# Performance work log

Measured on AMD Instinct MI355X. Metric: run time of the kernel, lower is better.

## Reference

```python
import jax, jax.numpy as jnp
import numpy as np

B, L, D = 256, 512, 768
ATTN_H, WIDTH_DIM = 1000, 20
BINS = jnp.array([1, 2, 3, 4, 5, 6, 7, 8, 12, 16, 20, 24, 32, 64, 128], dtype=jnp.int64)


def setup_inputs() -> dict:
    key = jax.random.key(0)
    ks = jax.random.split(key, 20)
    s = 0.02
    embeds = jax.random.normal(ks[0], (B, L, D), dtype=jnp.float32)
    spans = jnp.sort(jax.random.randint(ks[1], (B, 2), 0, L, dtype=jnp.int64), axis=1)
    inp = {
        "embeds": embeds,
        "spans": spans,
        # attention scorer: Linear(768,1000) -> LeakyReLU -> Linear(1000,1)
        "aw1": jax.random.normal(ks[2], (D, ATTN_H), dtype=jnp.float32) * s,
        "ab1": jnp.zeros((ATTN_H,), dtype=jnp.float32),
        "aw2": jax.random.normal(ks[3], (ATTN_H, 1), dtype=jnp.float32) * s,
        "ab2": jnp.zeros((1,), dtype=jnp.float32),
        # width embedding: [len(bins)+1 = 16, 20]
        "width_emb": jax.random.normal(ks[4], (16, WIDTH_DIM), dtype=jnp.float32) * s,
        # score MLP: 2324 -> 1024 -> 512 -> 256 -> 30
        "sw1": jax.random.normal(ks[5], (2324, 1024), dtype=jnp.float32) * s,
        "sb1": jnp.zeros((1024,), dtype=jnp.float32),
        "sw2": jax.random.normal(ks[6], (1024, 512), dtype=jnp.float32) * s,
        "sb2": jnp.zeros((512,), dtype=jnp.float32),
        "sw3": jax.random.normal(ks[7], (512, 256), dtype=jnp.float32) * s,
        "sb3": jnp.zeros((256,), dtype=jnp.float32),
        "sw4": jax.random.normal(ks[8], (256, 30), dtype=jnp.float32) * s,
        "sb4": jnp.zeros((30,), dtype=jnp.float32),
    }
    return inp


def reference(embeds, spans, aw1, ab1, aw2, ab2, width_emb,
              sw1, sb1, sw2, sb2, sw3, sb3, sw4, sb4):
    b, l, d = embeds.shape
    start, end = spans[:, 0], spans[:, 1]

    # gather start/end token embeds -> [B, 2*D]
    se = jnp.take_along_axis(embeds, spans[:, :, None], axis=1).reshape(b, 2 * d)

    # attention logits over all tokens: Linear -> LeakyReLU -> Linear
    h = jax.nn.leaky_relu(embeds @ aw1 + ab1)          # [B, L, 1000]
    attns = (h @ aw2 + ab2)[..., 0]                     # [B, L]

    # ragged per-span softmax pooling, vectorized via masking (inclusive span)
    cols = jnp.arange(l, dtype=spans.dtype)[None, :]
    mask = (cols >= start[:, None]) & (cols <= end[:, None])
    w = jax.nn.softmax(jnp.where(mask, attns, jnp.float32(-1e30)), axis=1)
    w = w * mask.astype(w.dtype)
    attn_embeds = jnp.einsum("bl,bld->bd", w, embeds)   # [B, D]

    # width bucket embedding
    widths = end - start + 1
    idx = jnp.sum(widths[:, None] > BINS[None, :], axis=1)
    wemb = width_emb[idx]                                # [B, 20]

    x = jnp.concatenate([se, attn_embeds, wemb], axis=1)  # [B, 2324]
    x = jax.nn.leaky_relu(x @ sw1 + sb1)
    x = jax.nn.leaky_relu(x @ sw2 + sb2)
    x = jax.nn.leaky_relu(x @ sw3 + sb3)
    return x @ sw4 + sb4                                  # [B, 30]
```

## Files before the change

### kernel.cpp

```cpp
#include <hip/hip_runtime.h>
#include <hip/hip_bf16.h>

#define B_   256
#define L_   512
#define D_   768
#define H_   1000
#define NPAD 1024
#define XDIM 2324
#define MAXPOS (B_*L_)

typedef _Float16 half8 __attribute__((ext_vector_type(8)));
typedef float    f32x4 __attribute__((ext_vector_type(4)));

__global__ __launch_bounds__(256) void scan_kernel(const int* __restrict__ spans,
                                                   int* __restrict__ meta) {
    int b = threadIdx.x;
    int s = spans[2 * b], e = spans[2 * b + 1];
    s = min(max(s, 0), L_ - 1);
    e = min(max(e, s), L_ - 1);
    int w = e - s + 1;
    __shared__ int sw[256];
    sw[b] = w;
    __syncthreads();
    for (int d = 1; d < 256; d <<= 1) {
        int v = 0;
        if (b >= d) v = sw[b - d];
        __syncthreads();
        if (b >= d) sw[b] += v;
        __syncthreads();
    }
    meta[b]       = sw[b] - w;
    meta[256 + b] = s;
    meta[512 + b] = e;
    if (b == 255) meta[768] = sw[255];
}

__global__ __launch_bounds__(256) void pos_fill(const int* __restrict__ meta,
                                                int* __restrict__ pos_list) {
    int b = blockIdx.x;
    int off = meta[b], start = meta[256 + b], end = meta[512 + b];
    int w = end - start + 1;
    for (int i = threadIdx.x; i < w; i += blockDim.x)
        pos_list[off + i] = (b << 16) | (start + i);
}

__global__ __launch_bounds__(256) void transpose_w(const float* __restrict__ aw1,
                                                   _Float16* __restrict__ WbT) {
    int k0 = blockIdx.x * 32, n0 = blockIdx.y * 32;
    int tx = threadIdx.x & 31, ty = threadIdx.x >> 5;
    __shared__ float T[32][33];
#pragma unroll
    for (int it = 0; it < 4; it++) {
        int k = k0 + ty + 8 * it;
        int n = n0 + tx;
        T[ty + 8 * it][tx] = (n < H_) ? aw1[(size_t)k * H_ + n] : 0.f;
    }
    __syncthreads();
#pragma unroll
    for (int it = 0; it < 4; it++) {
        int n = n0 + ty + 8 * it;
        WbT[(size_t)n * D_ + k0 + tx] = (_Float16)T[tx][ty + 8 * it];
    }
}

#define AP 776
__global__ __launch_bounds__(256) void attn_gemm_v2(
    const float* __restrict__ embeds, const _Float16* __restrict__ WbT,
    const float* __restrict__ ab1, const float* __restrict__ aw2,
    const int* __restrict__ pos_list, const int* __restrict__ meta,
    float* __restrict__ attns) {
    int npos = meta[768];
    int m0 = blockIdx.x * 32;
    if (m0 >= npos) return;
    int t = threadIdx.x;
    int lane = t & 63, w = t >> 6;
    int q = lane >> 4, l15 = lane & 15;

    __shared__ alignas(16) _Float16 As[32][AP];
    __shared__ unsigned rowoff[32];
    __shared__ float attns_s[4][32];

    if (t < 32) {
        unsigned off = 0;
        int m = m0 + t;
        if (m < npos) {
            int p = pos_list[m];
            off = (unsigned)((p >> 16) * (L_ * D_) + (p & 0xffff) * D_);
        }
        rowoff[t] = off;
    }
    __syncthreads();

    {
        int row = t >> 3;
        int cs = (t & 7) * 96;
        const float* src = embeds + rowoff[row] + cs;
#pragma unroll
        for (int i2 = 0; i2 < 12; i2++) {
            float4 v0 = *(const float4*)(src + i2 * 8);
            float4 v1 = *(const float4*)(src + i2 * 8 + 4);
            half8 h;
            h[0] = (_Float16)v0.x; h[1] = (_Float16)v0.y;
            h[2] = (_Float16)v0.z; h[3] = (_Float16)v0.w;
            h[4] = (_Float16)v1.x; h[5] = (_Float16)v1.y;
            h[6] = (_Float16)v1.z; h[7] = (_Float16)v1.w;
            *(half8*)&As[row][cs + i2 * 8] = h;
        }
    }
    __syncthreads();

    float pacc[2][4];
#pragma unroll
    for (int i = 0; i < 2; i++)
#pragma unroll
        for (int r = 0; r < 4; r++) pacc[i][r] = 0.f;

    for (int g = 0; g < 4; g++) {
        int colbase = w * 256 + g * 64;
        const _Float16* bbase = WbT + (size_t)(colbase + l15) * D_ + q * 8;
        f32x4 acc[2][4];
#pragma unroll
        for (int i = 0; i < 2; i++)
#pragma unroll
            for (int j = 0; j < 4; j++) acc[i][j] = (f32x4){0.f, 0.f, 0.f, 0.f};

        for (int k0 = 0; k0 < D_; k0 += 32) {
            half8 bf[4];
#pragma unroll
            for (int j = 0; j < 4; j++)
                bf[j] = *(const half8*)(bbase + (size_t)j * 16 * D_ + k0);
            half8 af[2];
#pragma unroll
            for (int i = 0; i < 2; i++)
                af[i] = *(const half8*)&As[l15 + 16 * i][k0 + q * 8];
#pragma unroll
            for (int i = 0; i < 2; i++)
#pragma unroll
                for (int j = 0; j < 4; j++)
                    acc[i][j] = __builtin_amdgcn_mfma_f32_16x16x32_f16(af[i], bf[j], acc[i][j], 0, 0, 0);
        }

        float bj[4], aj[4];
#pragma unroll
        for (int j = 0; j < 4; j++) {
            int col = colbase + j * 16 + l15;
            bool v = col < H_;
            bj[j] = v ? ab1[col] : 0.f;
            aj[j] = v ? aw2[col] : 0.f;
        }
#pragma unroll
        for (int i = 0; i < 2; i++) {
#pragma unroll
            for (int r = 0; r < 4; r++) {
                float p = 0.f;
#pragma unroll
                for (int j = 0; j < 4; j++) {
                    float h = acc[i][j][r] + bj[j];
                    h = h > 0.f ? h : 0.01f * h;
                    p += h * aj[j];
                }
                p += __shfl_xor(p, 1);
                p += __shfl_xor(p, 2);
                p += __shfl_xor(p, 4);
                p += __shfl_xor(p, 8);
                pacc[i][r] += p;
            }
        }
    }
    if (l15 == 0) {
#pragma unroll
        for (int i = 0; i < 2; i++)
#pragma unroll
            for (int r = 0; r < 4; r++)
                attns_s[w][i * 16 + q * 4 + r] = pacc[i][r];
    }
    __syncthreads();
    if (t < 32 && m0 + t < npos)
        attns[m0 + t] = attns_s[0][t] + attns_s[1][t] + attns_s[2][t] + attns_s[3][t];
}

__global__ __launch_bounds__(256) void build_x(
    const float* __restrict__ embeds, const float* __restrict__ attns,
    const int* __restrict__ meta, const float* __restrict__ width_emb,
    float* __restrict__ x) {
    int b = blockIdx.x, s = blockIdx.y, t = threadIdx.x;
    int off = meta[b], start = meta[256 + b], end = meta[512 + b];
    int w = end - start + 1;
    __shared__ float sv[512];
    __shared__ float red[256];
    for (int i = t; i < w; i += 256) sv[i] = attns[off + i];
    __syncthreads();
    float m = -3.0e38f;
    for (int i = t; i < w; i += 256) m = fmaxf(m, sv[i]);
    red[t] = m;
    __syncthreads();
    for (int st = 128; st > 0; st >>= 1) {
        if (t < st) red[t] = fmaxf(red[t], red[t + st]);
        __syncthreads();
    }
    float mx = red[0];
    __syncthreads();
    float ssum = 0.f;
    for (int i = t; i < w; i += 256) {
        float e = __expf(sv[i] - mx);
        sv[i] = e;
        ssum += e;
    }
    red[t] = ssum;
    __syncthreads();
    for (int st = 128; st > 0; st >>= 1) {
        if (t < st) red[t] += red[t + st];
        __syncthreads();
    }
    float inv = 1.0f / red[0];
    __syncthreads();

    int dim = s * 256 + t;
    const float* base = embeds + ((size_t)b * L_ + start) * D_ + dim;
    float acc = 0.f;
    int i = 0;
    for (; i + 3 < w; i += 4) {
        float w0 = sv[i], w1 = sv[i + 1], w2 = sv[i + 2], w3 = sv[i + 3];
        const float* p = base + (size_t)i * D_;
        acc += w0 * p[0] + w1 * p[D_] + w2 * p[2 * D_] + w3 * p[3 * D_];
    }
    for (; i < w; i++) acc += sv[i] * base[(size_t)i * D_];

    float* xb = x + (size_t)b * XDIM;
    xb[1536 + dim] = acc * inv;
    xb[dim]        = base[0];
    xb[768 + dim]  = embeds[((size_t)b * L_ + end) * D_ + dim];
    if (s == 0 && t < 20) {
        const int bins[15] = {1, 2, 3, 4, 5, 6, 7, 8, 12, 16, 20, 24, 32, 64, 128};
        int idx = 0;
#pragma unroll
        for (int q2 = 0; q2 < 15; q2++) idx += (w > bins[q2]);
        xb[2304 + t] = width_emb[idx * 20 + t];
    }
}

__global__ __launch_bounds__(256) void mlp_gemm_sk(
    const float* __restrict__ A, const float* __restrict__ W,
    float* __restrict__ out, int M, int N, int K, int kchunk) {
    __shared__ float As[16][68];
    __shared__ float Ws[16][64];
    int t = threadIdx.x;
    int tx = t & 15, ty = t >> 4;
    int m0 = blockIdx.x * 64, n0 = blockIdx.y * 64;
    int ks = blockIdx.z * kchunk;
    int ke = min(ks + kchunk, K);
    if (ks >= ke) return;
    int ar = t >> 2, akc = (t & 3) * 4;
    int wk = t >> 4, wnc = (t & 15) * 4;
    bool n4 = ((N & 3) == 0);

    float acc[4][4];
#pragma unroll
    for (int i = 0; i < 4; i++)
#pragma unroll
        for (int j = 0; j < 4; j++) acc[i][j] = 0.f;

    auto loadA = [&](int k0) -> float4 {
        float4 r = make_float4(0.f, 0.f, 0.f, 0.f);
        int k = k0 + akc;
        if (k < ke) r = *(const float4*)(A + (size_t)(m0 + ar) * K + k);
        return r;
    };
    auto loadW = [&](int k0) -> float4 {
        float4 r = make_float4(0.f, 0.f, 0.f, 0.f);
        int k = k0 + wk;
        if (k < ke) {
            int n = n0 + wnc;
            const float* p = W + (size_t)k * N + n;
            if (n4) {
                r = *(const float4*)p;
            } else {
                float tmp[4];
#pragma unroll
                for (int q2 = 0; q2 < 4; q2++)
                    tmp[q2] = (n + q2 < N) ? p[q2] : 0.f;
                r = make_float4(tmp[0], tmp[1], tmp[2], tmp[3]);
            }
        }
        return r;
    };

    float4 aR = loadA(ks), wR = loadW(ks);
    for (int k0 = ks; k0 < ke; k0 += 16) {
        As[akc + 0][ar] = aR.x;
        As[akc + 1][ar] = aR.y;
        As[akc + 2][ar] = aR.z;
        As[akc + 3][ar] = aR.w;
        *(float4*)&Ws[wk][wnc] = wR;
        __syncthreads();
        if (k0 + 16 < ke) { aR = loadA(k0 + 16); wR = loadW(k0 + 16); }
#pragma unroll
        for (int kk = 0; kk < 16; kk++) {
            float4 a = *(const float4*)&As[kk][ty * 4];
            float4 b = *(const float4*)&Ws[kk][tx * 4];
            float av[4] = {a.x, a.y, a.z, a.w};
            float bv[4] = {b.x, b.y, b.z, b.w};
#pragma unroll
            for (int i = 0; i < 4; i++)
#pragma unroll
                for (int j = 0; j < 4; j++) acc[i][j] += av[i] * bv[j];
        }
        __syncthreads();
    }
#pragma unroll
    for (int i = 0; i < 4; i++) {
#pragma unroll
        for (int j = 0; j < 4; j++) {
            int nn = n0 + tx * 4 + j;
            if (nn < N)
                atomicAdd(&out[(size_t)(m0 + ty * 4 + i) * N + nn], acc[i][j]);
        }
    }
}

__global__ __launch_bounds__(256) void bias_act(
    const float* __restrict__ src, const float* __restrict__ bias,
    float* __restrict__ dst, int total, int N, int leaky) {
    int i = blockIdx.x * 256 + threadIdx.x;
    int stride = gridDim.x * 256;
    for (; i < total; i += stride) {
        float v = src[i] + bias[i % N];
        if (leaky) v = v > 0.f ? v : 0.01f * v;
        dst[i] = v;
    }
}

extern "C" void kernel_launch(void* const* d_in, const int* in_sizes, int n_in,
                              void* d_out, int out_size, void* d_ws, size_t ws_size,
                              hipStream_t stream) {
    const float* embeds    = (const float*)d_in[0];
    const int*   spans     = (const int*)d_in[1];
    const float* aw1       = (const float*)d_in[2];
    const float* ab1       = (const float*)d_in[3];
    const float* aw2       = (const float*)d_in[4];
    const float* width_emb = (const float*)d_in[6];
    const float* sw1 = (const float*)d_in[7],  *sb1 = (const float*)d_in[8];
    const float* sw2 = (const float*)d_in[9],  *sb2 = (const float*)d_in[10];
    const float* sw3 = (const float*)d_in[11], *sb3 = (const float*)d_in[12];
    const float* sw4 = (const float*)d_in[13], *sb4 = (const float*)d_in[14];
    float* out = (float*)d_out;

    char* ws = (char*)d_ws;
    float*     attns    = (float*)ws;
    int*       pos_list = (int*)(ws + (size_t)MAXPOS * 4);
    int*       meta     = (int*)(ws + (size_t)MAXPOS * 8);
    _Float16*  WbT      = (_Float16*)(ws + (size_t)MAXPOS * 8 + 4096);
    float* x  = (float*)(ws + (size_t)MAXPOS * 8 + 4096 + (size_t)NPAD * D_ * 2);
    float* y1 = x + (size_t)B_ * XDIM;
    float* y2 = y1 + (size_t)B_ * 1024;
    float* y3 = y2 + (size_t)B_ * 512;
    float* y4 = y3 + (size_t)B_ * 256;
    size_t ybytes = ((size_t)B_ * (1024 + 512 + 256 + 30)) * 4;

    hipMemsetAsync(y1, 0, ybytes, stream);
    scan_kernel<<<1, 256, 0, stream>>>(spans, meta);
    pos_fill<<<B_, 256, 0, stream>>>(meta, pos_list);
    transpose_w<<<dim3(D_ / 32, NPAD / 32), 256, 0, stream>>>(aw1, WbT);
    attn_gemm_v2<<<MAXPOS / 32, 256, 0, stream>>>(
        embeds, WbT, ab1, aw2, pos_list, meta, attns);
    build_x<<<dim3(B_, 3), 256, 0, stream>>>(embeds, attns, meta, width_emb, x);

    mlp_gemm_sk<<<dim3(4, 16, 8), 256, 0, stream>>>(x,  sw1, y1, B_, 1024, XDIM, 292);
    bias_act<<<256, 256, 0, stream>>>(y1, sb1, y1, B_ * 1024, 1024, 1);
    mlp_gemm_sk<<<dim3(4, 8, 8), 256, 0, stream>>>(y1, sw2, y2, B_, 512, 1024, 128);
    bias_act<<<128, 256, 0, stream>>>(y2, sb2, y2, B_ * 512, 512, 1);
    mlp_gemm_sk<<<dim3(4, 4, 8), 256, 0, stream>>>(y2, sw3, y3, B_, 256, 512, 64);
    bias_act<<<64, 256, 0, stream>>>(y3, sb3, y3, B_ * 256, 256, 1);
    mlp_gemm_sk<<<dim3(4, 1, 8), 256, 0, stream>>>(y3, sw4, y4, B_, 30, 256, 32);
    bias_act<<<30, 256, 0, stream>>>(y4, sb4, out, B_ * 30, 30, 0);
}
```

Before: 901.7 us.

## Retile attention GEMM to 128x128 blocks with double-buffered LDS and direct global-to-LDS loads

The attention scorer GEMM changes from 32-row blocks that each sweep all 1024 hidden columns to 2D 128x128 tiles over positions and hidden columns. The K loop is double-buffered: weights go straight to LDS via global_load_lds, and embeds are converted to fp16 in registers. Per-tile partial logits are combined with atomicAdd into a zeroed attns buffer, replacing the old in-block reduction. This should raise reuse of B from LDS and improve MFMA utilization, at the cost of an extra memset, atomics, and re-reading A for each of the 8 column tiles.

```diff
diff --git a/kernel.cpp b/kernel.cpp
--- a/kernel.cpp
+++ b/kernel.cpp
@@ -63,24 +63,34 @@
     }
 }
 
-#define AP 776
-__global__ __launch_bounds__(256) void attn_gemm_v2(
+#define BM   128
+#define BN   128
+#define BKT  32
+#define NKST (D_ / BKT)
+
+#define GLD_LDS16(gsrc, ldst) \
+    __builtin_amdgcn_global_load_lds((const __attribute__((address_space(1))) void*)(gsrc), \
+                                     (__attribute__((address_space(3))) void*)(ldst), 16, 0, 0)
+
+__global__ __launch_bounds__(256) void attn_gemm_v3(
     const float* __restrict__ embeds, const _Float16* __restrict__ WbT,
     const float* __restrict__ ab1, const float* __restrict__ aw2,
     const int* __restrict__ pos_list, const int* __restrict__ meta,
     float* __restrict__ attns) {
     int npos = meta[768];
-    int m0 = blockIdx.x * 32;
+    int m0 = blockIdx.x * BM;
     if (m0 >= npos) return;
+    int n0 = blockIdx.y * BN;
     int t = threadIdx.x;
     int lane = t & 63, w = t >> 6;
     int q = lane >> 4, l15 = lane & 15;
-
-    __shared__ alignas(16) _Float16 As[32][AP];
-    __shared__ unsigned rowoff[32];
-    __shared__ float attns_s[4][32];
-
-    if (t < 32) {
+    int wr = w >> 1, wc = w & 1;
+
+    __shared__ alignas(16) _Float16 As[2][BM][BKT];
+    __shared__ alignas(16) _Float16 Bs[2][BN * BKT];
+    __shared__ unsigned rowoff[BM];
+
+    if (t < BM) {
         unsigned off = 0;
         int m = m0 + t;
         if (m < npos) {
@@ -91,92 +101,112 @@
     }
     __syncthreads();
 
-    {
-        int row = t >> 3;
-        int cs = (t & 7) * 96;
-        const float* src = embeds + rowoff[row] + cs;
-#pragma unroll
-        for (int i2 = 0; i2 < 12; i2++) {
-            float4 v0 = *(const float4*)(src + i2 * 8);
-            float4 v1 = *(const float4*)(src + i2 * 8 + 4);
-            half8 h;
-            h[0] = (_Float16)v0.x; h[1] = (_Float16)v0.y;
-            h[2] = (_Float16)v0.z; h[3] = (_Float16)v0.w;
-            h[4] = (_Float16)v1.x; h[5] = (_Float16)v1.y;
-            h[6] = (_Float16)v1.z; h[7] = (_Float16)v1.w;
-            *(half8*)&As[row][cs + i2 * 8] = h;
-        }
-    }
-    __syncthreads();
-
-    float pacc[2][4];
-#pragma unroll
-    for (int i = 0; i < 2; i++)
-#pragma unroll
-        for (int r = 0; r < 4; r++) pacc[i][r] = 0.f;
-
-    for (int g = 0; g < 4; g++) {
-        int colbase = w * 256 + g * 64;
-        const _Float16* bbase = WbT + (size_t)(colbase + l15) * D_ + q * 8;
-        f32x4 acc[2][4];
-#pragma unroll
-        for (int i = 0; i < 2; i++)
-#pragma unroll
-            for (int j = 0; j < 4; j++) acc[i][j] = (f32x4){0.f, 0.f, 0.f, 0.f};
-
-        for (int k0 = 0; k0 < D_; k0 += 32) {
-            half8 bf[4];
-#pragma unroll
-            for (int j = 0; j < 4; j++)
-                bf[j] = *(const half8*)(bbase + (size_t)j * 16 * D_ + k0);
-            half8 af[2];
-#pragma unroll
-            for (int i = 0; i < 2; i++)
-                af[i] = *(const half8*)&As[l15 + 16 * i][k0 + q * 8];
-#pragma unroll
-            for (int i = 0; i < 2; i++)
-#pragma unroll
-                for (int j = 0; j < 4; j++)
-                    acc[i][j] = __builtin_amdgcn_mfma_f32_16x16x32_f16(af[i], bf[j], acc[i][j], 0, 0, 0);
-        }
-
-        float bj[4], aj[4];
-#pragma unroll
-        for (int j = 0; j < 4; j++) {
-            int col = colbase + j * 16 + l15;
-            bool v = col < H_;
-            bj[j] = v ? ab1[col] : 0.f;
-            aj[j] = v ? aw2[col] : 0.f;
-        }
-#pragma unroll
-        for (int i = 0; i < 2; i++) {
-#pragma unroll
-            for (int r = 0; r < 4; r++) {
-                float p = 0.f;
-#pragma unroll
-                for (int j = 0; j < 4; j++) {
-                    float h = acc[i][j][r] + bj[j];
-                    h = h > 0.f ? h : 0.01f * h;
-                    p += h * aj[j];
-                }
-                p += __shfl_xor(p, 1);
-                p += __shfl_xor(p, 2);
-                p += __shfl_xor(p, 4);
-                p += __shfl_xor(p, 8);
-                pacc[i][r] += p;
+    const int arow = t >> 1;
+    const int acol = (t & 1) * 16;
+    const float* aptr = embeds + rowoff[arow] + acol;
+
+    const _Float16* bptr = WbT + (size_t)(n0 + (t >> 2)) * D_ + (t & 3) * 8;
+
+    float4 ar0, ar1, ar2, ar3;
+    auto loadA = [&](int k0) {
+        const float* p = aptr + k0;
+        ar0 = *(const float4*)(p + 0);
+        ar1 = *(const float4*)(p + 4);
+        ar2 = *(const float4*)(p + 8);
+        ar3 = *(const float4*)(p + 12);
+    };
+    auto writeA = [&](int bbuf) {
+        half8 h0, h1;
+        h0[0] = (_Float16)ar0.x; h0[1] = (_Float16)ar0.y;
+        h0[2] = (_Float16)ar0.z; h0[3] = (_Float16)ar0.w;
+        h0[4] = (_Float16)ar1.x; h0[5] = (_Float16)ar1.y;
+        h0[6] = (_Float16)ar1.z; h0[7] = (_Float16)ar1.w;
+        h1[0] = (_Float16)ar2.x; h1[1] = (_Float16)ar2.y;
+        h1[2] = (_Float16)ar2.z; h1[3] = (_Float16)ar2.w;
+        h1[4] = (_Float16)ar3.x; h1[5] = (_Float16)ar3.y;
+        h1[6] = (_Float16)ar3.z; h1[7] = (_Float16)ar3.w;
+        *(half8*)&As[bbuf][arow][acol]     = h0;
+        *(half8*)&As[bbuf][arow][acol + 8] = h1;
+    };
+    auto issueB = [&](int bbuf, int k0) {
+        const _Float16* s0 = bptr + k0;
+        _Float16* d0 = &Bs[bbuf][0] + w * 512;
+        GLD_LDS16(s0, d0);
+        const _Float16* s1 = s0 + (size_t)64 * D_;
+        _Float16* d1 = d0 + 2048;
+        GLD_LDS16(s1, d1);
+    };
+
+    f32x4 acc[4][4];
+#pragma unroll
+    for (int mi = 0; mi < 4; mi++)
+#pragma unroll
+        for (int ni = 0; ni < 4; ni++) acc[mi][ni] = (f32x4){0.f, 0.f, 0.f, 0.f};
+
+    auto compute = [&](int bbuf) {
+        half8 af[4], bf[4];
+#pragma unroll
+        for (int mi = 0; mi < 4; mi++)
+            af[mi] = *(const half8*)&As[bbuf][wr * 64 + mi * 16 + l15][q * 8];
+#pragma unroll
+        for (int ni = 0; ni < 4; ni++)
+            bf[ni] = *(const half8*)&Bs[bbuf][((wc * 64 + ni * 16 + l15) << 5) + q * 8];
+#pragma unroll
+        for (int mi = 0; mi < 4; mi++)
+#pragma unroll
+            for (int ni = 0; ni < 4; ni++)
+                acc[mi][ni] = __builtin_amdgcn_mfma_f32_16x16x32_f16(
+                    af[mi], bf[ni], acc[mi][ni], 0, 0, 0);
+    };
+
+    issueB(0, 0);
+    loadA(0);
+    writeA(0);
+    __syncthreads();
+
+    int buf = 0;
+#pragma unroll 2
+    for (int ks = 0; ks < NKST - 1; ks++) {
+        int kn = (ks + 1) * BKT;
+        issueB(buf ^ 1, kn);
+        loadA(kn);
+        compute(buf);
+        writeA(buf ^ 1);
+        __syncthreads();
+        buf ^= 1;
+    }
+    compute(buf);
+
+    int colb = n0 + wc * 64;
+    float bj[4], aj[4];
+#pragma unroll
+    for (int ni = 0; ni < 4; ni++) {
+        int col = colb + ni * 16 + l15;
+        bool v = col < H_;
+        bj[ni] = v ? ab1[col] : 0.f;
+        aj[ni] = v ? aw2[col] : 0.f;
+    }
+#pragma unroll
+    for (int mi = 0; mi < 4; mi++) {
+#pragma unroll
+        for (int r = 0; r < 4; r++) {
+            float p = 0.f;
+#pragma unroll
+            for (int ni = 0; ni < 4; ni++) {
+                float h = acc[mi][ni][r] + bj[ni];
+                h = h > 0.f ? h : 0.01f * h;
+                p += h * aj[ni];
+            }
+            p += __shfl_xor(p, 1);
+            p += __shfl_xor(p, 2);
+            p += __shfl_xor(p, 4);
+            p += __shfl_xor(p, 8);
+            if (l15 == 0) {
+                int row = m0 + wr * 64 + mi * 16 + q * 4 + r;
+                if (row < npos) atomicAdd(&attns[row], p);
             }
         }
     }
-    if (l15 == 0) {
-#pragma unroll
-        for (int i = 0; i < 2; i++)
-#pragma unroll
-            for (int r = 0; r < 4; r++)
-                attns_s[w][i * 16 + q * 4 + r] = pacc[i][r];
-    }
-    __syncthreads();
-    if (t < 32 && m0 + t < npos)
-        attns[m0 + t] = attns_s[0][t] + attns_s[1][t] + attns_s[2][t] + attns_s[3][t];
 }
 
 __global__ __launch_bounds__(256) void build_x(
@@ -358,10 +388,11 @@
     size_t ybytes = ((size_t)B_ * (1024 + 512 + 256 + 30)) * 4;
 
     hipMemsetAsync(y1, 0, ybytes, stream);
+    hipMemsetAsync(attns, 0, (size_t)MAXPOS * 4, stream);
     scan_kernel<<<1, 256, 0, stream>>>(spans, meta);
     pos_fill<<<B_, 256, 0, stream>>>(meta, pos_list);
     transpose_w<<<dim3(D_ / 32, NPAD / 32), 256, 0, stream>>>(aw1, WbT);
-    attn_gemm_v2<<<MAXPOS / 32, 256, 0, stream>>>(
+    attn_gemm_v3<<<dim3(MAXPOS / BM, NPAD / BN), 256, 0, stream>>>(
         embeds, WbT, ab1, aw2, pos_list, meta, attns);
     build_x<<<dim3(B_, 3), 256, 0, stream>>>(embeds, attns, meta, width_emb, x);
 
```

After: 801.6 us. 1.12x faster.
